# Performance work log

Measured on AMD Instinct MI355X. Metric: run time of the kernel, lower is better.

The kernel has to match this reference:

```python
import jax, jax.numpy as jnp
import numpy as np

B, C, K = 8192, 4096, 4096
BK, BN = 1, 16          # block-sparse tile sizes (bk x bn)
KEEP = 0.3


def setup_inputs() -> dict:
    key = jax.random.key(0)
    kx, kw, kb, km = jax.random.split(key, 4)
    stdv = 1.0 / np.sqrt(C * K)  # reset_parameters uses 1/sqrt(C*K)
    x = jax.random.normal(kx, (B, C), dtype=jnp.float32)
    weight = jax.random.uniform(kw, (K, C), dtype=jnp.float32, minval=-stdv, maxval=stdv)
    # block mask on (K/bk, C/bn) grid, expanded to full weight shape
    blk = (jax.random.uniform(km, (K // BK, C // BN)) < KEEP).astype(jnp.float32)
    mask = jnp.repeat(jnp.repeat(blk, BK, axis=0), BN, axis=1)  # [K, C]
    weight = weight * mask
    bias = jax.random.uniform(kb, (K,), dtype=jnp.float32, minval=-stdv, maxval=stdv)
    return {"x": x, "weight": weight, "bias": bias}


def reference(x, weight, bias):
    # SparseLinearRelu forward (sparse-kernel path, attr='relu'):
    # y = relu(x @ W^T + b); zero blocks of W contribute nothing (skipped by kernel).
    return jax.nn.relu(jnp.dot(x, weight.T) + bias)
```

## Files before the change

kernel.cpp:

```cpp
#include <hip/hip_runtime.h>
#include <hip/hip_bf16.h>

typedef __attribute__((ext_vector_type(4))) float f32x4;
typedef __attribute__((ext_vector_type(8))) short bf16x8;
typedef __attribute__((ext_vector_type(4))) short bf16x4v;

#define M_DIM 8192
#define N_DIM 4096
#define K_DIM 4096
#define NX (M_DIM * K_DIM)
#define NW (N_DIM * K_DIM)

#define BM 256
#define BN 256
#define BK 64
#define NKT (K_DIM / BK)
#define THREADS 512

#define GLOAD_LDS16(g, l)                                                        \
  __builtin_amdgcn_global_load_lds(                                              \
      (const __attribute__((address_space(1))) void*)(g),                        \
      (__attribute__((address_space(3))) void*)(l), 16, 0, 0)

__global__ __launch_bounds__(256) void convert_bf16(const float* __restrict__ x,
                                                    const float* __restrict__ w,
                                                    short* __restrict__ ws) {
  const long stride = (long)gridDim.x * blockDim.x;
  const long total8 = ((long)NX + NW) / 8;
  for (long i = blockIdx.x * (long)blockDim.x + threadIdx.x; i < total8; i += stride) {
    const long base = i * 8;
    const float* src = (base < NX) ? (x + base) : (w + (base - NX));
    short* dst = ws + base;
    f32x4 a = *(const f32x4*)src;
    f32x4 b = *(const f32x4*)(src + 4);
    bf16x8 o;
    o[0] = (short)__bfloat16_as_ushort(__float2bfloat16(a[0]));
    o[1] = (short)__bfloat16_as_ushort(__float2bfloat16(a[1]));
    o[2] = (short)__bfloat16_as_ushort(__float2bfloat16(a[2]));
    o[3] = (short)__bfloat16_as_ushort(__float2bfloat16(a[3]));
    o[4] = (short)__bfloat16_as_ushort(__float2bfloat16(b[0]));
    o[5] = (short)__bfloat16_as_ushort(__float2bfloat16(b[1]));
    o[6] = (short)__bfloat16_as_ushort(__float2bfloat16(b[2]));
    o[7] = (short)__bfloat16_as_ushort(__float2bfloat16(b[3]));
    *(bf16x8*)dst = o;
  }
}

__global__ __launch_bounds__(THREADS, 2) void gemm256_bf16(
    const short* __restrict__ Abf,
    const short* __restrict__ Bbf,
    const float* __restrict__ bias,
    float* __restrict__ Y) {
  __shared__ short lds[2 * 32768];
  char* const ldsb = (char*)lds;

  const int tid  = threadIdx.x;
  const int lane = tid & 63;
  const int wave = tid >> 6;
  const int wm   = wave >> 2;
  const int wn   = wave & 3;

  const int lin = blockIdx.x + blockIdx.y * (N_DIM / BN);
  const int swz = (lin & 7) * 64 + (lin >> 3);
  const int bx = swz & 15;
  const int by = swz >> 4;
  const long rowA0 = (long)by * BM;
  const long rowB0 = (long)bx * BN;

  const int sg_col = (((lane & 7) ^ ((lane >> 3) & 7)) << 3);
  const int s_row  = wave * 8 + (lane >> 3);

  const short* gA = Abf + (rowA0 + s_row) * (long)K_DIM + sg_col;
  const short* gB = Bbf + (rowB0 + s_row) * (long)K_DIM + sg_col;

  const int offk0 = (lane & 15) * 128 + ((((lane >> 4)) ^ (lane & 7)) << 4);
  const int offk1 = (lane & 15) * 128 + (((4 + (lane >> 4)) ^ (lane & 7)) << 4);

#define STAGE_A(BOFF_, TT) do {                                                  \
    const short* g_ = gA + (long)(TT) * BK;                                      \
    _Pragma("unroll")                                                            \
    for (int is_ = 0; is_ < 4; ++is_)                                            \
      GLOAD_LDS16(g_ + (long)is_ * 64 * K_DIM,                                   \
                  ldsb + (BOFF_) + is_ * 8192 + wave * 1024);                    \
  } while (0)

#define STAGE_B(BOFF_, TT) do {                                                  \
    const short* g_ = gB + (long)(TT) * BK;                                      \
    _Pragma("unroll")                                                            \
    for (int is_ = 0; is_ < 4; ++is_)                                            \
      GLOAD_LDS16(g_ + (long)is_ * 64 * K_DIM,                                   \
                  ldsb + (BOFF_) + 32768 + is_ * 8192 + wave * 1024);            \
  } while (0)

#define PH_READ_A(DST, BOFF_, MADD) do {                                         \
    const char* pa_ = ldsb + (BOFF_) + wm * 16384 + (MADD);                      \
    _Pragma("unroll")                                                            \
    for (int m_ = 0; m_ < 4; ++m_) {                                             \
      DST[m_][0] = *(const bf16x8*)(pa_ + m_ * 2048 + offk0);                    \
      DST[m_][1] = *(const bf16x8*)(pa_ + m_ * 2048 + offk1);                    \
    }                                                                            \
  } while (0)

#define PH_READ_B(DST, BOFF_, NADD) do {                                         \
    const char* pb_ = ldsb + (BOFF_) + 32768 + wn * 8192 + (NADD);               \
    _Pragma("unroll")                                                            \
    for (int n_ = 0; n_ < 2; ++n_) {                                             \
      DST[n_][0] = *(const bf16x8*)(pb_ + n_ * 2048 + offk0);                    \
      DST[n_][1] = *(const bf16x8*)(pb_ + n_ * 2048 + offk1);                    \
    }                                                                            \
  } while (0)

#define MFMA16(AF, BF, MB, NB) do {                                              \
    __builtin_amdgcn_s_setprio(1);                                               \
    _Pragma("unroll")                                                            \
    for (int kk_ = 0; kk_ < 2; ++kk_)                                            \
      _Pragma("unroll")                                                          \
      for (int m_ = 0; m_ < 4; ++m_)                                             \
        _Pragma("unroll")                                                        \
        for (int n_ = 0; n_ < 2; ++n_)                                           \
          acc[(MB) + m_][(NB) + n_] = __builtin_amdgcn_mfma_f32_16x16x32_bf16(   \
              AF[m_][kk_], BF[n_][kk_], acc[(MB) + m_][(NB) + n_], 0, 0, 0);     \
    __builtin_amdgcn_s_setprio(0);                                               \
  } while (0)

#define TILE(CUR, ALT, BOFF_, NOFF_, T, DO_ST, DO_PF, VM8) do {                  \
                              \
    asm volatile("s_waitcnt lgkmcnt(0)" ::: "memory");                           \
    __builtin_amdgcn_sched_barrier(0);                                           \
    PH_READ_A(ALT, BOFF_, 8192);                                                 \
    __builtin_amdgcn_sched_barrier(0);                                           \
    MFMA16(CUR, bfr01, 0, 0);                                                    \
    __builtin_amdgcn_s_barrier();                                                \
                               \
    asm volatile("s_waitcnt lgkmcnt(0)" ::: "memory");                           \
    __builtin_amdgcn_sched_barrier(0);                                           \
    PH_READ_B(bfr23, BOFF_, 4096);                                               \
    __builtin_amdgcn_sched_barrier(0);                                           \
    MFMA16(ALT, bfr01, 4, 0);                                                    \
    __builtin_amdgcn_s_barrier();                                                \
                                  \
    asm volatile("s_waitcnt lgkmcnt(0)" ::: "memory");                           \
    __builtin_amdgcn_sched_barrier(0);                                           \
    if (DO_ST) STAGE_A(BOFF_, (T) + 2);                                          \
    __builtin_amdgcn_sched_barrier(0);                                           \
    MFMA16(ALT, bfr23, 4, 2);                                                    \
    __builtin_amdgcn_s_barrier();                                                \
         \
                 \
    if (DO_ST) STAGE_B(BOFF_, (T) + 2);                                          \
    if (DO_PF) {                                                                 \
      if (VM8) asm volatile("s_waitcnt vmcnt(8)" ::: "memory");                  \
      else     asm volatile("s_waitcnt vmcnt(0)" ::: "memory");                  \
      __builtin_amdgcn_s_barrier();                                              \
      __builtin_amdgcn_sched_barrier(0);                                         \
      PH_READ_A(ALT, NOFF_, 0);                                                  \
      PH_READ_B(bfr01, NOFF_, 0);                                                \
      __builtin_amdgcn_sched_barrier(0);                                         \
    }                                                                            \
    MFMA16(CUR, bfr23, 0, 2);                                                    \
  } while (0)

  f32x4 acc[8][4];
#pragma unroll
  for (int i = 0; i < 8; ++i)
#pragma unroll
    for (int j = 0; j < 4; ++j) acc[i][j] = (f32x4)0.0f;

  bf16x8 afA[4][2], afB[4][2], bfr01[2][2], bfr23[2][2];

  STAGE_A(0, 0);
  STAGE_B(0, 0);
  STAGE_A(65536, 1);
  STAGE_B(65536, 1);
  asm volatile("s_waitcnt vmcnt(8)" ::: "memory");
  __builtin_amdgcn_s_barrier();
  __builtin_amdgcn_sched_barrier(0);
  PH_READ_A(afA, 0, 0);
  PH_READ_B(bfr01, 0, 0);
  __builtin_amdgcn_sched_barrier(0);

  for (int tp = 0; tp < NKT / 2 - 1; ++tp) {
    const int t0 = 2 * tp;
    TILE(afA, afB, 0, 65536, t0, 1, 1, 1);
    TILE(afB, afA, 65536, 0, t0 + 1, 1, 1, 1);
  }
  TILE(afA, afB, 0, 65536, NKT - 2, 0, 1, 0);
  TILE(afB, afA, 65536, 0, NKT - 1, 0, 0, 0);

#undef TILE
#undef MFMA16
#undef PH_READ_B
#undef PH_READ_A
#undef STAGE_B
#undef STAGE_A

  const int c0 = lane & 15;
  const int r0 = (lane >> 4) * 4;
#pragma unroll
  for (int j = 0; j < 4; ++j) {
    const long gc = rowB0 + wn * 64 + j * 16 + c0;
    const float bv = bias[gc];
#pragma unroll
    for (int i = 0; i < 8; ++i) {
      const long gr0 = rowA0 + wm * 128 + i * 16 + r0;
#pragma unroll
      for (int r = 0; r < 4; ++r) {
        float v = acc[i][j][r] + bv;
        Y[(gr0 + r) * (long)N_DIM + gc] = fmaxf(v, 0.0f);
      }
    }
  }
}

#define FBM 128
#define FBK 32
#define FLDSS 40
__global__ __launch_bounds__(256) void fallback_gemm(
    const float* __restrict__ X, const float* __restrict__ W,
    const float* __restrict__ bias, float* __restrict__ Y) {
  __shared__ short As[FBM * FLDSS];
  __shared__ short Bs[FBM * FLDSS];
  const int tid = threadIdx.x, lane = tid & 63, wave = tid >> 6;
  const int wm = (wave >> 1) * 64, wn = (wave & 1) * 64;
  const long rowA0 = (long)blockIdx.y * FBM, rowB0 = (long)blockIdx.x * FBM;
  const int srow = tid >> 3, scol = (tid & 7) * 4;
  const float* Aptr = X + (rowA0 + srow) * (long)K_DIM + scol;
  const float* Bptr = W + (rowB0 + srow) * (long)K_DIM + scol;
  f32x4 ra[4], rb[4];
#pragma unroll
  for (int i = 0; i < 4; ++i) {
    ra[i] = *(const f32x4*)(Aptr + (long)i * 32 * K_DIM);
    rb[i] = *(const f32x4*)(Bptr + (long)i * 32 * K_DIM);
  }
  f32x4 acc[4][4];
#pragma unroll
  for (int i = 0; i < 4; ++i)
#pragma unroll
    for (int j = 0; j < 4; ++j) acc[i][j] = (f32x4)0.0f;
  for (int kt = 0; kt < K_DIM / FBK; ++kt) {
    __syncthreads();
#pragma unroll
    for (int i = 0; i < 4; ++i) {
      bf16x4v pa, pb;
#pragma unroll
      for (int j = 0; j < 4; ++j) {
        pa[j] = (short)__bfloat16_as_ushort(__float2bfloat16(ra[i][j]));
        pb[j] = (short)__bfloat16_as_ushort(__float2bfloat16(rb[i][j]));
      }
      *(bf16x4v*)&As[(i * 32 + srow) * FLDSS + scol] = pa;
      *(bf16x4v*)&Bs[(i * 32 + srow) * FLDSS + scol] = pb;
    }
    if (kt + 1 < K_DIM / FBK) {
      const float* An = Aptr + (kt + 1) * FBK;
      const float* Bn = Bptr + (kt + 1) * FBK;
#pragma unroll
      for (int i = 0; i < 4; ++i) {
        ra[i] = *(const f32x4*)(An + (long)i * 32 * K_DIM);
        rb[i] = *(const f32x4*)(Bn + (long)i * 32 * K_DIM);
      }
    }
    __syncthreads();
    bf16x8 af[4], bfr[4];
#pragma unroll
    for (int i = 0; i < 4; ++i) {
      af[i]  = *(const bf16x8*)&As[(wm + i * 16 + (lane & 15)) * FLDSS + (lane >> 4) * 8];
      bfr[i] = *(const bf16x8*)&Bs[(wn + i * 16 + (lane & 15)) * FLDSS + (lane >> 4) * 8];
    }
#pragma unroll
    for (int i = 0; i < 4; ++i)
#pragma unroll
      for (int j = 0; j < 4; ++j)
        acc[i][j] = __builtin_amdgcn_mfma_f32_16x16x32_bf16(af[i], bfr[j], acc[i][j], 0, 0, 0);
  }
  const int r0 = (lane >> 4) * 4, c0 = lane & 15;
#pragma unroll
  for (int j = 0; j < 4; ++j) {
    const long gc = rowB0 + wn + j * 16 + c0;
    const float bv = bias[gc];
#pragma unroll
    for (int i = 0; i < 4; ++i) {
      const long gr0 = rowA0 + wm + i * 16 + r0;
#pragma unroll
      for (int r = 0; r < 4; ++r) {
        float v = acc[i][j][r] + bv;
        Y[(gr0 + r) * (long)N_DIM + gc] = fmaxf(v, 0.0f);
      }
    }
  }
}

extern "C" void kernel_launch(void* const* d_in, const int* in_sizes, int n_in,
                              void* d_out, int out_size, void* d_ws, size_t ws_size,
                              hipStream_t stream) {
  const float* x = (const float*)d_in[0];
  const float* w = (const float*)d_in[1];
  const float* b = (const float*)d_in[2];
  float* y = (float*)d_out;

  const size_t need = (size_t)(NX + NW) * sizeof(short);
  if (ws_size >= need) {
    short* ws = (short*)d_ws;
    convert_bf16<<<2048, 256, 0, stream>>>(x, w, ws);
    dim3 grid(N_DIM / BN, M_DIM / BM);
    gemm256_bf16<<<grid, dim3(THREADS), 0, stream>>>(ws, ws + NX, b, y);
  } else {
    dim3 grid(N_DIM / FBM, M_DIM / FBM);
    fallback_gemm<<<grid, dim3(256), 0, stream>>>(x, w, b, y);
  }
}
```

Baseline: 281.8 us.

## Restructure GEMM pipeline into half-tile staged loads with single fragment set

```diff
diff --git a/kernel.cpp b/kernel.cpp
--- a/kernel.cpp
+++ b/kernel.cpp
@@ -69,27 +69,21 @@
 
   const int sg_col = (((lane & 7) ^ ((lane >> 3) & 7)) << 3);
   const int s_row  = wave * 8 + (lane >> 3);
-
-  const short* gA = Abf + (rowA0 + s_row) * (long)K_DIM + sg_col;
-  const short* gB = Bbf + (rowB0 + s_row) * (long)K_DIM + sg_col;
+  const int voff = s_row * K_DIM + sg_col;
+
+  const short* uA = Abf + rowA0 * (long)K_DIM;
+  const short* uB = Bbf + rowB0 * (long)K_DIM;
 
   const int offk0 = (lane & 15) * 128 + ((((lane >> 4)) ^ (lane & 7)) << 4);
   const int offk1 = (lane & 15) * 128 + (((4 + (lane >> 4)) ^ (lane & 7)) << 4);
 
-#define STAGE_A(BOFF_, TT) do {                                                  \
-    const short* g_ = gA + (long)(TT) * BK;                                      \
-    _Pragma("unroll")                                                            \
-    for (int is_ = 0; is_ < 4; ++is_)                                            \
-      GLOAD_LDS16(g_ + (long)is_ * 64 * K_DIM,                                   \
-                  ldsb + (BOFF_) + is_ * 8192 + wave * 1024);                    \
-  } while (0)
-
-#define STAGE_B(BOFF_, TT) do {                                                  \
-    const short* g_ = gB + (long)(TT) * BK;                                      \
-    _Pragma("unroll")                                                            \
-    for (int is_ = 0; is_ < 4; ++is_)                                            \
-      GLOAD_LDS16(g_ + (long)is_ * 64 * K_DIM,                                   \
-                  ldsb + (BOFF_) + 32768 + is_ * 8192 + wave * 1024);            \
+#define STAGE_HALF(BOFF_, HALF_, TT) do {                                        \
+    const short* u_ = ((HALF_) < 2 ? uA : uB) +                                  \
+                      (long)(((HALF_) & 1) * 128) * K_DIM + (long)(TT) * BK;     \
+    char* l_ = ldsb + (BOFF_) + ((HALF_) < 2 ? 0 : 32768) +                      \
+               ((HALF_) & 1) * 16384 + wave * 1024;                              \
+    GLOAD_LDS16(u_ + voff, l_);                                                  \
+    GLOAD_LDS16(u_ + 64 * K_DIM + voff, l_ + 8192);                              \
   } while (0)
 
 #define PH_READ_A(DST, BOFF_, MADD) do {                                         \
@@ -123,41 +117,29 @@
     __builtin_amdgcn_s_setprio(0);                                               \
   } while (0)
 
-#define TILE(CUR, ALT, BOFF_, NOFF_, T, DO_ST, DO_PF, VM8) do {                  \
-                              \
-    asm volatile("s_waitcnt lgkmcnt(0)" ::: "memory");                           \
-    __builtin_amdgcn_sched_barrier(0);                                           \
-    PH_READ_A(ALT, BOFF_, 8192);                                                 \
-    __builtin_amdgcn_sched_barrier(0);                                           \
-    MFMA16(CUR, bfr01, 0, 0);                                                    \
+#define TILE(BOFF_, OOFF_, T, VM) do {                                           \
+              \
+    PH_READ_A(af, BOFF_, 0);                                                     \
+    PH_READ_B(bfr01, BOFF_, 0);                                                  \
+    if ((T) + 1 < NKT) STAGE_HALF(OOFF_, 1, (T) + 1);                            \
+    MFMA16(af, bfr01, 0, 0);                                                     \
     __builtin_amdgcn_s_barrier();                                                \
-                               \
-    asm volatile("s_waitcnt lgkmcnt(0)" ::: "memory");                           \
-    __builtin_amdgcn_sched_barrier(0);                                           \
+                       \
     PH_READ_B(bfr23, BOFF_, 4096);                                               \
-    __builtin_amdgcn_sched_barrier(0);                                           \
-    MFMA16(ALT, bfr01, 4, 0);                                                    \
+    if ((T) + 1 < NKT) STAGE_HALF(OOFF_, 3, (T) + 1);                            \
+    MFMA16(af, bfr23, 0, 2);                                                     \
     __builtin_amdgcn_s_barrier();                                                \
-                                  \
-    asm volatile("s_waitcnt lgkmcnt(0)" ::: "memory");                           \
-    __builtin_amdgcn_sched_barrier(0);                                           \
-    if (DO_ST) STAGE_A(BOFF_, (T) + 2);                                          \
-    __builtin_amdgcn_sched_barrier(0);                                           \
-    MFMA16(ALT, bfr23, 4, 2);                                                    \
+                                        \
+    PH_READ_A(af, BOFF_, 8192);                                                  \
+    MFMA16(af, bfr01, 4, 0);                                                     \
     __builtin_amdgcn_s_barrier();                                                \
-         \
-                 \
-    if (DO_ST) STAGE_B(BOFF_, (T) + 2);                                          \
-    if (DO_PF) {                                                                 \
-      if (VM8) asm volatile("s_waitcnt vmcnt(8)" ::: "memory");                  \
-      else     asm volatile("s_waitcnt vmcnt(0)" ::: "memory");                  \
-      __builtin_amdgcn_s_barrier();                                              \
-      __builtin_amdgcn_sched_barrier(0);                                         \
-      PH_READ_A(ALT, NOFF_, 0);                                                  \
-      PH_READ_B(bfr01, NOFF_, 0);                                                \
-      __builtin_amdgcn_sched_barrier(0);                                         \
-    }                                                                            \
-    MFMA16(CUR, bfr23, 0, 2);                                                    \
+                \
+    if ((T) + 2 < NKT) { STAGE_HALF(BOFF_, 0, (T) + 2);                          \
+                         STAGE_HALF(BOFF_, 2, (T) + 2); }                        \
+    MFMA16(af, bfr23, 4, 2);                                                     \
+    if ((VM) == 4)      asm volatile("s_waitcnt vmcnt(4)" ::: "memory");         \
+    else if ((VM) == 0) asm volatile("s_waitcnt vmcnt(0)" ::: "memory");         \
+    if ((VM) >= 0) __builtin_amdgcn_s_barrier();                                 \
   } while (0)
 
   f32x4 acc[8][4];
@@ -166,33 +148,30 @@
 #pragma unroll
     for (int j = 0; j < 4; ++j) acc[i][j] = (f32x4)0.0f;
 
-  bf16x8 afA[4][2], afB[4][2], bfr01[2][2], bfr23[2][2];
-
-  STAGE_A(0, 0);
-  STAGE_B(0, 0);
-  STAGE_A(65536, 1);
-  STAGE_B(65536, 1);
-  asm volatile("s_waitcnt vmcnt(8)" ::: "memory");
+  bf16x8 af[4][2], bfr01[2][2], bfr23[2][2];
+
+  STAGE_HALF(0, 0, 0);
+  STAGE_HALF(0, 1, 0);
+  STAGE_HALF(0, 2, 0);
+  STAGE_HALF(0, 3, 0);
+  STAGE_HALF(65536, 0, 1);
+  STAGE_HALF(65536, 2, 1);
+  asm volatile("s_waitcnt vmcnt(4)" ::: "memory");
   __builtin_amdgcn_s_barrier();
-  __builtin_amdgcn_sched_barrier(0);
-  PH_READ_A(afA, 0, 0);
-  PH_READ_B(bfr01, 0, 0);
-  __builtin_amdgcn_sched_barrier(0);
 
   for (int tp = 0; tp < NKT / 2 - 1; ++tp) {
     const int t0 = 2 * tp;
-    TILE(afA, afB, 0, 65536, t0, 1, 1, 1);
-    TILE(afB, afA, 65536, 0, t0 + 1, 1, 1, 1);
-  }
-  TILE(afA, afB, 0, 65536, NKT - 2, 0, 1, 0);
-  TILE(afB, afA, 65536, 0, NKT - 1, 0, 0, 0);
+    TILE(0,     65536, t0,     4);
+    TILE(65536, 0,     t0 + 1, 4);
+  }
+  TILE(0,     65536, NKT - 2, 0);
+  TILE(65536, 0,     NKT - 1, -1);
 
 #undef TILE
 #undef MFMA16
 #undef PH_READ_B
 #undef PH_READ_A
-#undef STAGE_B
-#undef STAGE_A
+#undef STAGE_HALF
 
   const int c0 = lane & 15;
   const int r0 = (lane >> 4) * 4;
```

After: 264.4 us. 6.2% less time.
